# Kernel optimization log

Measured on AMD Instinct MI355X. Metric: run time of the kernel, lower is better.

Reference implementation:

```python
import jax, jax.numpy as jnp
import numpy as np

EMBED = 768
HEADS = 12
HDIM = EMBED // HEADS
FF = EMBED * 2
B, LQ, LK = 4, 2048, 2048


def _linear(x, W, b):
    # W: [in, out]
    return x @ W + b


def _layernorm(x, g, b, eps=1e-5):
    mu = jnp.mean(x, axis=-1, keepdims=True)
    var = jnp.mean(jnp.square(x - mu), axis=-1, keepdims=True)
    return (x - mu) * jax.lax.rsqrt(var + eps) * g + b


def _l2norm(x, eps=1e-12):
    # matches F.normalize: x / max(||x||_2, eps)
    n = jnp.sqrt(jnp.sum(jnp.square(x), axis=-1, keepdims=True))
    return x / jnp.maximum(n, eps)


def _heads(x):
    b, l, _ = x.shape
    return x.reshape(b, l, HEADS, HDIM).transpose(0, 2, 1, 3)  # [B,H,L,hd]


def setup_inputs() -> dict:
    key = jax.random.key(0)
    ks = jax.random.split(key, 20)
    s = 0.02
    d = {
        'image_tokens': jax.random.normal(ks[0], (B, LQ, EMBED), jnp.float32),
        'point_tokens': jax.random.normal(ks[1], (B, LK, EMBED), jnp.float32),
        'image_pos': jax.random.normal(ks[2], (B, LQ, EMBED), jnp.float32),
        'point_pos': jax.random.normal(ks[3], (B, LK, EMBED), jnp.float32),
        'Wip': jax.random.normal(ks[4], (EMBED, EMBED), jnp.float32) * s,
        'bip': jnp.zeros((EMBED,), jnp.float32),
        'Wpp': jax.random.normal(ks[5], (EMBED, EMBED), jnp.float32) * s,
        'bpp': jnp.zeros((EMBED,), jnp.float32),
        'Wq': jax.random.normal(ks[6], (EMBED, EMBED), jnp.float32) * s,
        'bq': jnp.zeros((EMBED,), jnp.float32),
        'Wk': jax.random.normal(ks[7], (EMBED, EMBED), jnp.float32) * s,
        'bk': jnp.zeros((EMBED,), jnp.float32),
        'Wv': jax.random.normal(ks[8], (EMBED, EMBED), jnp.float32) * s,
        'bv': jnp.zeros((EMBED,), jnp.float32),
        'Wo': jax.random.normal(ks[9], (EMBED, EMBED), jnp.float32) * s,
        'bo': jnp.zeros((EMBED,), jnp.float32),
        'g1': jnp.ones((EMBED,), jnp.float32),
        'b1': jnp.zeros((EMBED,), jnp.float32),
        'g2': jnp.ones((EMBED,), jnp.float32),
        'b2': jnp.zeros((EMBED,), jnp.float32),
        'Wf1': jax.random.normal(ks[10], (EMBED, FF), jnp.float32) * s,
        'bf1': jnp.zeros((FF,), jnp.float32),
        'Wf2': jax.random.normal(ks[11], (FF, EMBED), jnp.float32) * s,
        'bf2': jnp.zeros((EMBED,), jnp.float32),
    }
    return d


def reference(image_tokens, point_tokens, image_pos, point_pos,
              Wip, bip, Wpp, bpp, Wq, bq, Wk, bk, Wv, bv, Wo, bo,
              g1, b1, g2, b2, Wf1, bf1, Wf2, bf2):
    q = _linear(image_tokens + _linear(image_pos, Wip, bip), Wq, bq)
    k = _linear(point_tokens + _linear(point_pos, Wpp, bpp), Wk, bk)
    v = _linear(point_tokens, Wv, bv)

    q = _l2norm(_heads(q))  # [B,H,Lq,hd]
    k = _l2norm(_heads(k))  # [B,H,Lk,hd]
    v = _heads(v)           # [B,H,Lk,hd]

    scores = jnp.einsum('bhqd,bhkd->bhqk', q, k)
    attn = jax.nn.softmax(scores, axis=-1)
    fused = jnp.einsum('bhqk,bhkd->bhqd', attn, v)
    fused = fused.transpose(0, 2, 1, 3).reshape(image_tokens.shape[0], image_tokens.shape[1], EMBED)

    fused = _layernorm(image_tokens + _linear(fused, Wo, bo), g1, b1)
    h = _linear(fused, Wf1, bf1)
    h = 0.5 * h * (1.0 + jax.lax.erf(h / jnp.sqrt(jnp.float32(2.0))))  # exact GELU
    ff = _linear(h, Wf2, bf2)
    return _layernorm(fused + ff, g2, b2)
```

## Files before the change

kernel.cpp:

```cpp
#include <hip/hip_runtime.h>

#define EMBED 768
#define FFDIM 1536
#define BATCH 4
#define SEQ   2048
#define HEADS 12
#define MROWS (BATCH*SEQ)

typedef __attribute__((ext_vector_type(4))) float  f32x4;
typedef __attribute__((ext_vector_type(8))) __bf16 bf16x8;
typedef __attribute__((ext_vector_type(4))) short  s16x4;

__device__ __forceinline__ short f2bf(float f) {
    union { float f; unsigned u; } x; x.f = f;
    unsigned r = x.u + 0x7fffu + ((x.u >> 16) & 1u);
    return (short)(r >> 16);
}

__device__ __forceinline__ void gll16(const void* g, void* l) {
    __builtin_amdgcn_global_load_lds(
        (const __attribute__((address_space(1))) void*)g,
        (__attribute__((address_space(3))) void*)l, 16, 0, 0);
}

__global__ __launch_bounds__(256) void cvt4_kernel(
    const float* __restrict__ s0, const float* __restrict__ s1,
    const float* __restrict__ s2, const float* __restrict__ s3,
    short* __restrict__ o0, short* __restrict__ o1,
    short* __restrict__ o2, short* __restrict__ o3)
{
    const float* s; short* o;
    switch (blockIdx.y) {
        case 0:  s = s0; o = o0; break;
        case 1:  s = s1; o = o1; break;
        case 2:  s = s2; o = o2; break;
        default: s = s3; o = o3; break;
    }
    size_t i = ((size_t)blockIdx.x * 256 + threadIdx.x) * 4;
    float4 v = *(const float4*)(s + i);
    s16x4 r;
    r[0] = f2bf(v.x); r[1] = f2bf(v.y); r[2] = f2bf(v.z); r[3] = f2bf(v.w);
    *(s16x4*)(o + i) = r;
}

__global__ __launch_bounds__(256) void transpose_w(
    const float* __restrict__ W, short* __restrict__ Wt, int K, int N)
{
    __shared__ float tile[32][33];
    const int k0 = blockIdx.y * 32, n0 = blockIdx.x * 32;
    const int tx = threadIdx.x & 31, ty = threadIdx.x >> 5;
    #pragma unroll
    for (int i = 0; i < 32; i += 8)
        tile[ty + i][tx] = W[(size_t)(k0 + ty + i) * N + n0 + tx];
    __syncthreads();
    #pragma unroll
    for (int i = 0; i < 32; i += 8)
        Wt[(size_t)(n0 + ty + i) * K + k0 + tx] = f2bf(tile[tx][ty + i]);
}

__global__ __launch_bounds__(256) void transpose_v(
    const short* __restrict__ v, short* __restrict__ vt)
{
    __shared__ short tile[64][65];
    const int bh = blockIdx.y;
    const int b = bh / HEADS, h = bh % HEADS;
    const int k0 = blockIdx.x * 64;
    const int tx = threadIdx.x & 63, ty = threadIdx.x >> 6;
    #pragma unroll
    for (int i = 0; i < 64; i += 4)
        tile[ty + i][tx] = v[(size_t)(b * SEQ + k0 + ty + i) * EMBED + h * 64 + tx];
    __syncthreads();
    #pragma unroll
    for (int i = 0; i < 64; i += 4)
        vt[(size_t)(bh * 64 + ty + i) * SEQ + k0 + tx] = tile[tx][ty + i];
}

template<int L2N, int GELU_, int RES, int SBF, int SF32>
__global__ __launch_bounds__(256) void gemm_bt(
    const short* __restrict__ A, const short* __restrict__ Wt,
    const float* __restrict__ bias, const float* __restrict__ resid,
    short* __restrict__ outb, float* __restrict__ outf,
    int M, int N, int K)
{
    __shared__ short As[128][32];
    __shared__ short Bs[128][32];
    const int tid = threadIdx.x;
    const int mbase = blockIdx.y * 128, nbase = blockIdx.x * 128;
    const int wid = tid >> 6, lane = tid & 63;
    const int wm = wid >> 1, wn = wid & 1;
    const int l15 = lane & 15, lhi = lane >> 4;
    const int sr = tid >> 2;
    const int sc = (tid & 3) * 8;

    f32x4 acc[4][4] = {};

    const short* Ab = A  + (size_t)mbase * K;
    const short* Bb = Wt + (size_t)nbase * K;

    for (int k0 = 0; k0 < K; k0 += 32) {
        __syncthreads();
        gll16(Ab + (size_t)sr * K        + k0 + sc, &As[sr][sc]);
        gll16(Ab + (size_t)(64 + sr) * K + k0 + sc, &As[64 + sr][sc]);
        gll16(Bb + (size_t)sr * K        + k0 + sc, &Bs[sr][sc]);
        gll16(Bb + (size_t)(64 + sr) * K + k0 + sc, &Bs[64 + sr][sc]);
        __syncthreads();
        bf16x8 av[4], bv[4];
        #pragma unroll
        for (int t = 0; t < 4; ++t) {
            av[t] = *(const bf16x8*)(&As[wm * 64 + t * 16 + l15][lhi * 8]);
            bv[t] = *(const bf16x8*)(&Bs[wn * 64 + t * 16 + l15][lhi * 8]);
        }
        #pragma unroll
        for (int mt = 0; mt < 4; ++mt)
            #pragma unroll
            for (int nt = 0; nt < 4; ++nt)
                acc[mt][nt] = __builtin_amdgcn_mfma_f32_16x16x32_bf16(
                    av[mt], bv[nt], acc[mt][nt], 0, 0, 0);
    }

    #pragma unroll
    for (int mt = 0; mt < 4; ++mt) {
        float vals[4][4];
        #pragma unroll
        for (int nt = 0; nt < 4; ++nt) {
            const int col = nbase + wn * 64 + nt * 16 + l15;
            const float bc = bias[col];
            #pragma unroll
            for (int j = 0; j < 4; ++j) vals[nt][j] = acc[mt][nt][j] + bc;
        }
        if (RES) {
            #pragma unroll
            for (int nt = 0; nt < 4; ++nt) {
                const int col = nbase + wn * 64 + nt * 16 + l15;
                #pragma unroll
                for (int j = 0; j < 4; ++j) {
                    const int row = mbase + wm * 64 + mt * 16 + lhi * 4 + j;
                    vals[nt][j] += resid[(size_t)row * N + col];
                }
            }
        }
        if (L2N) {
            #pragma unroll
            for (int j = 0; j < 4; ++j) {
                float s = 0.f;
                #pragma unroll
                for (int nt = 0; nt < 4; ++nt) s += vals[nt][j] * vals[nt][j];
                s += __shfl_xor(s, 1); s += __shfl_xor(s, 2);
                s += __shfl_xor(s, 4); s += __shfl_xor(s, 8);
                const float inv = 1.0f / fmaxf(sqrtf(s), 1e-12f);
                #pragma unroll
                for (int nt = 0; nt < 4; ++nt) vals[nt][j] *= inv;
            }
        }
        if (GELU_) {
            #pragma unroll
            for (int nt = 0; nt < 4; ++nt)
                #pragma unroll
                for (int j = 0; j < 4; ++j) {
                    const float v = vals[nt][j];
                    vals[nt][j] = 0.5f * v * (1.0f + erff(v * 0.70710678118654752f));
                }
        }
        #pragma unroll
        for (int nt = 0; nt < 4; ++nt) {
            const int col = nbase + wn * 64 + nt * 16 + l15;
            #pragma unroll
            for (int j = 0; j < 4; ++j) {
                const int row = mbase + wm * 64 + mt * 16 + lhi * 4 + j;
                if (SBF)  outb[(size_t)row * N + col] = f2bf(vals[nt][j]);
                if (SF32) outf[(size_t)row * N + col] = vals[nt][j];
            }
        }
    }
}

__global__ __launch_bounds__(256) void attn_kernel(
    const short* __restrict__ qn, const short* __restrict__ kn,
    const short* __restrict__ vt, short* __restrict__ outp)
{
    __shared__ short Qs[64][64];
    __shared__ short Ks[64][64];
    __shared__ short Vs[64][64];
    __shared__ short Ps[64][64];

    const int bh = blockIdx.y;
    const int b = bh / HEADS, h = bh % HEADS;
    const int q0 = blockIdx.x * 64;
    const int tid = threadIdx.x, wid = tid >> 6, lane = tid & 63;
    const int l15 = lane & 15, lhi = lane >> 4;
    const int sr = tid >> 3;
    const int sc = (tid & 7) * 8;

    #pragma unroll
    for (int p = 0; p < 2; ++p) {
        const int r = p * 32 + sr;
        gll16(qn + (size_t)(b * SEQ + q0 + r) * EMBED + h * 64 + sc, &Qs[r][sc]);
    }

    f32x4 acc_o[4] = {};
    float rowsum[4] = {0.f, 0.f, 0.f, 0.f};

    for (int kt = 0; kt < SEQ / 64; ++kt) {
        const int k0 = kt * 64;
        __syncthreads();
        #pragma unroll
        for (int p = 0; p < 2; ++p) {
            const int r = p * 32 + sr;
            gll16(kn + (size_t)(b * SEQ + k0 + r) * EMBED + h * 64 + sc, &Ks[r][sc]);
            gll16(vt + (size_t)(bh * 64 + r) * SEQ + k0 + sc, &Vs[r][sc]);
        }
        __syncthreads();

        bf16x8 aq0 = *(const bf16x8*)(&Qs[wid * 16 + l15][lhi * 8]);
        bf16x8 aq1 = *(const bf16x8*)(&Qs[wid * 16 + l15][32 + lhi * 8]);
        #pragma unroll
        for (int nt = 0; nt < 4; ++nt) {
            bf16x8 bk0 = *(const bf16x8*)(&Ks[nt * 16 + l15][lhi * 8]);
            bf16x8 bk1 = *(const bf16x8*)(&Ks[nt * 16 + l15][32 + lhi * 8]);
            f32x4 s = {0.f, 0.f, 0.f, 0.f};
            s = __builtin_amdgcn_mfma_f32_16x16x32_bf16(aq0, bk0, s, 0, 0, 0);
            s = __builtin_amdgcn_mfma_f32_16x16x32_bf16(aq1, bk1, s, 0, 0, 0);
            #pragma unroll
            for (int j = 0; j < 4; ++j) {
                const float e = __expf(s[j]);
                rowsum[j] += e;
                Ps[wid * 16 + lhi * 4 + j][nt * 16 + l15] = f2bf(e);
            }
        }
        __syncthreads();

        #pragma unroll
        for (int ks = 0; ks < 2; ++ks) {
            bf16x8 ap = *(const bf16x8*)(&Ps[wid * 16 + l15][ks * 32 + lhi * 8]);
            #pragma unroll
            for (int dt = 0; dt < 4; ++dt) {
                bf16x8 bvv = *(const bf16x8*)(&Vs[dt * 16 + l15][ks * 32 + lhi * 8]);
                acc_o[dt] = __builtin_amdgcn_mfma_f32_16x16x32_bf16(ap, bvv, acc_o[dt], 0, 0, 0);
            }
        }
    }

    #pragma unroll
    for (int j = 0; j < 4; ++j) {
        float s = rowsum[j];
        s += __shfl_xor(s, 1); s += __shfl_xor(s, 2);
        s += __shfl_xor(s, 4); s += __shfl_xor(s, 8);
        rowsum[j] = s;
    }

    #pragma unroll
    for (int dt = 0; dt < 4; ++dt)
        #pragma unroll
        for (int j = 0; j < 4; ++j) {
            const int row = q0 + wid * 16 + lhi * 4 + j;
            const int col = h * 64 + dt * 16 + l15;
            outp[(size_t)(b * SEQ + row) * EMBED + col] = f2bf(acc_o[dt][j] / rowsum[j]);
        }
}

template<int SBF>
__global__ __launch_bounds__(256) void layernorm_768(
    const float* __restrict__ x, const float* __restrict__ g, const float* __restrict__ bb,
    float* __restrict__ outf, short* __restrict__ outb)
{
    const int row = blockIdx.x;
    const float* xr = x + (size_t)row * EMBED;
    const int t = threadIdx.x;
    const float v0 = xr[t], v1 = xr[t + 256], v2 = xr[t + 512];
    float s = v0 + v1 + v2;
    #pragma unroll
    for (int m = 1; m < 64; m <<= 1) s += __shfl_xor(s, m);
    __shared__ float red[4];
    __shared__ float red2[4];
    const int wid = t >> 6, lane = t & 63;
    if (lane == 0) red[wid] = s;
    __syncthreads();
    const float mu = (red[0] + red[1] + red[2] + red[3]) * (1.0f / 768.0f);
    const float d0 = v0 - mu, d1 = v1 - mu, d2 = v2 - mu;
    float ss = d0 * d0 + d1 * d1 + d2 * d2;
    #pragma unroll
    for (int m = 1; m < 64; m <<= 1) ss += __shfl_xor(ss, m);
    if (lane == 0) red2[wid] = ss;
    __syncthreads();
    const float var = (red2[0] + red2[1] + red2[2] + red2[3]) * (1.0f / 768.0f);
    const float inv = rsqrtf(var + 1e-5f);
    const float y0 = d0 * inv * g[t] + bb[t];
    const float y1 = d1 * inv * g[t + 256] + bb[t + 256];
    const float y2 = d2 * inv * g[t + 512] + bb[t + 512];
    float* of = outf + (size_t)row * EMBED;
    of[t] = y0; of[t + 256] = y1; of[t + 512] = y2;
    if (SBF) {
        short* ob = outb + (size_t)row * EMBED;
        ob[t] = f2bf(y0); ob[t + 256] = f2bf(y1); ob[t + 512] = f2bf(y2);
    }
}

extern "C" void kernel_launch(void* const* d_in, const int* in_sizes, int n_in,
                              void* d_out, int out_size, void* d_ws, size_t ws_size,
                              hipStream_t stream)
{
    (void)in_sizes; (void)n_in; (void)out_size; (void)ws_size;
    const float* itok = (const float*)d_in[0];
    const float* ptok = (const float*)d_in[1];
    const float* ipos = (const float*)d_in[2];
    const float* ppos = (const float*)d_in[3];
    const float* Wip = (const float*)d_in[4];  const float* bip = (const float*)d_in[5];
    const float* Wpp = (const float*)d_in[6];  const float* bpp = (const float*)d_in[7];
    const float* Wq  = (const float*)d_in[8];  const float* bq  = (const float*)d_in[9];
    const float* Wk  = (const float*)d_in[10]; const float* bk  = (const float*)d_in[11];
    const float* Wv  = (const float*)d_in[12]; const float* bv  = (const float*)d_in[13];
    const float* Wo  = (const float*)d_in[14]; const float* bo  = (const float*)d_in[15];
    const float* g1  = (const float*)d_in[16]; const float* b1  = (const float*)d_in[17];
    const float* g2  = (const float*)d_in[18]; const float* b2  = (const float*)d_in[19];
    const float* Wf1 = (const float*)d_in[20]; const float* bf1 = (const float*)d_in[21];
    const float* Wf2 = (const float*)d_in[22]; const float* bf2 = (const float*)d_in[23];
    float* out = (float*)d_out;

    char* ws = (char*)d_ws;
    constexpr size_t SZ_BF  = (size_t)MROWS * EMBED * 2;
    constexpr size_t SZ_F32 = (size_t)MROWS * EMBED * 4;
    constexpr size_t W768B  = (size_t)EMBED * EMBED * 2;
    constexpr size_t W1536B = (size_t)EMBED * FFDIM * 2;

    size_t o = 0;
    short* it_bf    = (short*)(ws + o); o += SZ_BF;
    short* pt_bf    = (short*)(ws + o); o += SZ_BF;
    short* ip_bf    = (short*)(ws + o); o += SZ_BF;
    short* pp_bf    = (short*)(ws + o); o += SZ_BF;
    short* qin_bf   = (short*)(ws + o); o += SZ_BF;
    short* kin_bf   = (short*)(ws + o); o += SZ_BF;
    short* qn_bf    = (short*)(ws + o); o += SZ_BF;
    short* kn_bf    = (short*)(ws + o); o += SZ_BF;
    short* attn_bf  = (short*)(ws + o); o += SZ_BF;
    float* x_f32    = (float*)(ws + o); o += SZ_F32;
    short* fused_bf = (short*)(ws + o); o += SZ_BF;
    float* fused_f32= (float*)(ws + o); o += SZ_F32;
    short* wip_t = (short*)(ws + o); o += W768B;
    short* wpp_t = (short*)(ws + o); o += W768B;
    short* wq_t  = (short*)(ws + o); o += W768B;
    short* wk_t  = (short*)(ws + o); o += W768B;
    short* wv_t  = (short*)(ws + o); o += W768B;
    short* wo_t  = (short*)(ws + o); o += W768B;
    short* wf1_t = (short*)(ws + o); o += W1536B;
    short* wf2_t = (short*)(ws + o); o += W1536B;
    short* v_bf  = ip_bf;
    short* vt_bf = pp_bf;
    short* h_bf  = qin_bf;

    const dim3 blk(256);

    cvt4_kernel<<<dim3(MROWS * EMBED / 1024, 4), blk, 0, stream>>>(
        itok, ptok, ipos, ppos, it_bf, pt_bf, ip_bf, pp_bf);

    transpose_w<<<dim3(EMBED / 32, EMBED / 32), blk, 0, stream>>>(Wip, wip_t, EMBED, EMBED);
    transpose_w<<<dim3(EMBED / 32, EMBED / 32), blk, 0, stream>>>(Wpp, wpp_t, EMBED, EMBED);
    transpose_w<<<dim3(EMBED / 32, EMBED / 32), blk, 0, stream>>>(Wq,  wq_t,  EMBED, EMBED);
    transpose_w<<<dim3(EMBED / 32, EMBED / 32), blk, 0, stream>>>(Wk,  wk_t,  EMBED, EMBED);
    transpose_w<<<dim3(EMBED / 32, EMBED / 32), blk, 0, stream>>>(Wv,  wv_t,  EMBED, EMBED);
    transpose_w<<<dim3(EMBED / 32, EMBED / 32), blk, 0, stream>>>(Wo,  wo_t,  EMBED, EMBED);
    transpose_w<<<dim3(FFDIM / 32, EMBED / 32), blk, 0, stream>>>(Wf1, wf1_t, EMBED, FFDIM);
    transpose_w<<<dim3(EMBED / 32, FFDIM / 32), blk, 0, stream>>>(Wf2, wf2_t, FFDIM, EMBED);

    const dim3 g768(EMBED / 128, MROWS / 128);
    const dim3 g1536(FFDIM / 128, MROWS / 128);

    gemm_bt<0,0,1,1,0><<<g768, blk, 0, stream>>>(ip_bf, wip_t, bip, itok, qin_bf, nullptr, MROWS, EMBED, EMBED);
    gemm_bt<0,0,1,1,0><<<g768, blk, 0, stream>>>(pp_bf, wpp_t, bpp, ptok, kin_bf, nullptr, MROWS, EMBED, EMBED);
    gemm_bt<1,0,0,1,0><<<g768, blk, 0, stream>>>(qin_bf, wq_t, bq, nullptr, qn_bf, nullptr, MROWS, EMBED, EMBED);
    gemm_bt<1,0,0,1,0><<<g768, blk, 0, stream>>>(kin_bf, wk_t, bk, nullptr, kn_bf, nullptr, MROWS, EMBED, EMBED);
    gemm_bt<0,0,0,1,0><<<g768, blk, 0, stream>>>(pt_bf, wv_t, bv, nullptr, v_bf, nullptr, MROWS, EMBED, EMBED);

    transpose_v<<<dim3(SEQ / 64, BATCH * HEADS), blk, 0, stream>>>(v_bf, vt_bf);
    attn_kernel<<<dim3(SEQ / 64, BATCH * HEADS), blk, 0, stream>>>(qn_bf, kn_bf, vt_bf, attn_bf);

    gemm_bt<0,0,1,0,1><<<g768, blk, 0, stream>>>(attn_bf, wo_t, bo, itok, nullptr, x_f32, MROWS, EMBED, EMBED);
    layernorm_768<1><<<dim3(MROWS), blk, 0, stream>>>(x_f32, g1, b1, fused_f32, fused_bf);
    gemm_bt<0,1,0,1,0><<<g1536, blk, 0, stream>>>(fused_bf, wf1_t, bf1, nullptr, h_bf, nullptr, MROWS, FFDIM, EMBED);
    gemm_bt<0,0,1,0,1><<<g768, blk, 0, stream>>>(h_bf, wf2_t, bf2, fused_f32, nullptr, x_f32, MROWS, EMBED, FFDIM);
    layernorm_768<0><<<dim3(MROWS), blk, 0, stream>>>(x_f32, g2, b2, out, nullptr);
}
```

Before: 640.5 us.

## Double-buffer GEMM and attention LDS tiles and swizzle attention shared memory

The GEMM main loop now keeps two LDS stages and prefetches the next K slice while computing the current one, with one barrier per iteration instead of two. The attention kernel moves to 512 threads handling 128 query rows per block. It double-buffers the K and V tiles, hoists the Q fragments out of the loop, and drops the barrier around the per-wave P tile. Attention LDS accesses for Q, K, V and P use an XOR chunk swizzle meant to avoid bank conflicts. The cost is twice the LDS footprint per block and correctness that depends on the async global-to-LDS loads finishing before each barrier.

```diff
diff --git a/kernel.cpp b/kernel.cpp
--- a/kernel.cpp
+++ b/kernel.cpp
@@ -23,6 +23,10 @@
         (__attribute__((address_space(3))) void*)l, 16, 0, 0);
 }
 
+__device__ __forceinline__ bf16x8 ldsw(const short* base, int row, int chunk) {
+    return *(const bf16x8*)((const char*)base + row * 128 + (((chunk ^ (row & 7))) << 4));
+}
+
 __global__ __launch_bounds__(256) void cvt4_kernel(
     const float* __restrict__ s0, const float* __restrict__ s1,
     const float* __restrict__ s2, const float* __restrict__ s3,
@@ -82,8 +86,8 @@
     short* __restrict__ outb, float* __restrict__ outf,
     int M, int N, int K)
 {
-    __shared__ short As[128][32];
-    __shared__ short Bs[128][32];
+    __shared__ short As[2][128][32];
+    __shared__ short Bs[2][128][32];
     const int tid = threadIdx.x;
     const int mbase = blockIdx.y * 128, nbase = blockIdx.x * 128;
     const int wid = tid >> 6, lane = tid & 63;
@@ -97,18 +101,24 @@
     const short* Ab = A  + (size_t)mbase * K;
     const short* Bb = Wt + (size_t)nbase * K;
 
-    for (int k0 = 0; k0 < K; k0 += 32) {
-        __syncthreads();
-        gll16(Ab + (size_t)sr * K        + k0 + sc, &As[sr][sc]);
-        gll16(Ab + (size_t)(64 + sr) * K + k0 + sc, &As[64 + sr][sc]);
-        gll16(Bb + (size_t)sr * K        + k0 + sc, &Bs[sr][sc]);
-        gll16(Bb + (size_t)(64 + sr) * K + k0 + sc, &Bs[64 + sr][sc]);
-        __syncthreads();
+#define GSTAGE(buf, kk)                                                         \
+    gll16(Ab + (size_t)sr * K        + (kk) + sc, &As[buf][sr][sc]);            \
+    gll16(Ab + (size_t)(64 + sr) * K + (kk) + sc, &As[buf][64 + sr][sc]);       \
+    gll16(Bb + (size_t)sr * K        + (kk) + sc, &Bs[buf][sr][sc]);            \
+    gll16(Bb + (size_t)(64 + sr) * K + (kk) + sc, &Bs[buf][64 + sr][sc]);
+
+    GSTAGE(0, 0);
+    __syncthreads();
+
+    const int nk = K >> 5;
+    for (int t = 0; t < nk; ++t) {
+        const int cur = t & 1;
+        if (t + 1 < nk) { GSTAGE(cur ^ 1, (t + 1) << 5); }
         bf16x8 av[4], bv[4];
         #pragma unroll
-        for (int t = 0; t < 4; ++t) {
-            av[t] = *(const bf16x8*)(&As[wm * 64 + t * 16 + l15][lhi * 8]);
-            bv[t] = *(const bf16x8*)(&Bs[wn * 64 + t * 16 + l15][lhi * 8]);
+        for (int tt = 0; tt < 4; ++tt) {
+            av[tt] = *(const bf16x8*)(&As[cur][wm * 64 + tt * 16 + l15][lhi * 8]);
+            bv[tt] = *(const bf16x8*)(&Bs[cur][wn * 64 + tt * 16 + l15][lhi * 8]);
         }
         #pragma unroll
         for (int mt = 0; mt < 4; ++mt)
@@ -116,7 +126,9 @@
             for (int nt = 0; nt < 4; ++nt)
                 acc[mt][nt] = __builtin_amdgcn_mfma_f32_16x16x32_bf16(
                     av[mt], bv[nt], acc[mt][nt], 0, 0, 0);
-    }
+        __syncthreads();
+    }
+#undef GSTAGE
 
     #pragma unroll
     for (int mt = 0; mt < 4; ++mt) {
@@ -174,49 +186,57 @@
     }
 }
 
-__global__ __launch_bounds__(256) void attn_kernel(
+__global__ __launch_bounds__(512) void attn_kernel(
     const short* __restrict__ qn, const short* __restrict__ kn,
     const short* __restrict__ vt, short* __restrict__ outp)
 {
-    __shared__ short Qs[64][64];
-    __shared__ short Ks[64][64];
-    __shared__ short Vs[64][64];
-    __shared__ short Ps[64][64];
+    __shared__ short Qs[128][64];
+    __shared__ short Ks[2][64][64];
+    __shared__ short Vs[2][64][64];
+    __shared__ short Ps[128][64];
 
     const int bh = blockIdx.y;
     const int b = bh / HEADS, h = bh % HEADS;
-    const int q0 = blockIdx.x * 64;
+    const int q0 = blockIdx.x * 128;
     const int tid = threadIdx.x, wid = tid >> 6, lane = tid & 63;
     const int l15 = lane & 15, lhi = lane >> 4;
-    const int sr = tid >> 3;
-    const int sc = (tid & 7) * 8;
+    const int srow = tid >> 3;
+    const int schk = tid & 7;
 
     #pragma unroll
     for (int p = 0; p < 2; ++p) {
-        const int r = p * 32 + sr;
-        gll16(qn + (size_t)(b * SEQ + q0 + r) * EMBED + h * 64 + sc, &Qs[r][sc]);
-    }
+        const int cid = p * 512 + tid;
+        const int r = cid >> 3, c = cid & 7;
+        gll16(qn + (size_t)(b * SEQ + q0 + r) * EMBED + h * 64 + ((c ^ (r & 7)) * 8),
+              &Qs[r][c * 8]);
+    }
+    gll16(kn + (size_t)(b * SEQ + srow) * EMBED + h * 64 + ((schk ^ (srow & 7)) * 8),
+          &Ks[0][srow][schk * 8]);
+    gll16(vt + (size_t)(bh * 64 + srow) * SEQ + ((schk ^ (srow & 7)) * 8),
+          &Vs[0][srow][schk * 8]);
+    __syncthreads();
+
+    const bf16x8 aq0 = ldsw(&Qs[0][0], wid * 16 + l15, lhi);
+    const bf16x8 aq1 = ldsw(&Qs[0][0], wid * 16 + l15, 4 + lhi);
 
     f32x4 acc_o[4] = {};
     float rowsum[4] = {0.f, 0.f, 0.f, 0.f};
+    char* const ps_base = (char*)&Ps[0][0];
 
     for (int kt = 0; kt < SEQ / 64; ++kt) {
-        const int k0 = kt * 64;
-        __syncthreads();
-        #pragma unroll
-        for (int p = 0; p < 2; ++p) {
-            const int r = p * 32 + sr;
-            gll16(kn + (size_t)(b * SEQ + k0 + r) * EMBED + h * 64 + sc, &Ks[r][sc]);
-            gll16(vt + (size_t)(bh * 64 + r) * SEQ + k0 + sc, &Vs[r][sc]);
-        }
-        __syncthreads();
-
-        bf16x8 aq0 = *(const bf16x8*)(&Qs[wid * 16 + l15][lhi * 8]);
-        bf16x8 aq1 = *(const bf16x8*)(&Qs[wid * 16 + l15][32 + lhi * 8]);
+        const int cur = kt & 1;
+        if (kt + 1 < SEQ / 64) {
+            const int k0n = (kt + 1) * 64;
+            gll16(kn + (size_t)(b * SEQ + k0n + srow) * EMBED + h * 64 + ((schk ^ (srow & 7)) * 8),
+                  &Ks[cur ^ 1][srow][schk * 8]);
+            gll16(vt + (size_t)(bh * 64 + srow) * SEQ + k0n + ((schk ^ (srow & 7)) * 8),
+                  &Vs[cur ^ 1][srow][schk * 8]);
+        }
+
         #pragma unroll
         for (int nt = 0; nt < 4; ++nt) {
-            bf16x8 bk0 = *(const bf16x8*)(&Ks[nt * 16 + l15][lhi * 8]);
-            bf16x8 bk1 = *(const bf16x8*)(&Ks[nt * 16 + l15][32 + lhi * 8]);
+            bf16x8 bk0 = ldsw(&Ks[cur][0][0], nt * 16 + l15, lhi);
+            bf16x8 bk1 = ldsw(&Ks[cur][0][0], nt * 16 + l15, 4 + lhi);
             f32x4 s = {0.f, 0.f, 0.f, 0.f};
             s = __builtin_amdgcn_mfma_f32_16x16x32_bf16(aq0, bk0, s, 0, 0, 0);
             s = __builtin_amdgcn_mfma_f32_16x16x32_bf16(aq1, bk1, s, 0, 0, 0);
@@ -224,20 +244,23 @@
             for (int j = 0; j < 4; ++j) {
                 const float e = __expf(s[j]);
                 rowsum[j] += e;
-                Ps[wid * 16 + lhi * 4 + j][nt * 16 + l15] = f2bf(e);
+                const int q = wid * 16 + lhi * 4 + j;
+                const int k = nt * 16 + l15;
+                const int chunk = k >> 3;
+                *(short*)(ps_base + q * 128 + ((chunk ^ (q & 7)) << 4) + (k & 7) * 2) = f2bf(e);
             }
         }
-        __syncthreads();
 
         #pragma unroll
         for (int ks = 0; ks < 2; ++ks) {
-            bf16x8 ap = *(const bf16x8*)(&Ps[wid * 16 + l15][ks * 32 + lhi * 8]);
+            bf16x8 ap = ldsw(&Ps[0][0], wid * 16 + l15, ks * 4 + lhi);
             #pragma unroll
             for (int dt = 0; dt < 4; ++dt) {
-                bf16x8 bvv = *(const bf16x8*)(&Vs[dt * 16 + l15][ks * 32 + lhi * 8]);
+                bf16x8 bvv = ldsw(&Vs[cur][0][0], dt * 16 + l15, ks * 4 + lhi);
                 acc_o[dt] = __builtin_amdgcn_mfma_f32_16x16x32_bf16(ap, bvv, acc_o[dt], 0, 0, 0);
             }
         }
+        __syncthreads();
     }
 
     #pragma unroll
@@ -371,7 +394,7 @@
     gemm_bt<0,0,0,1,0><<<g768, blk, 0, stream>>>(pt_bf, wv_t, bv, nullptr, v_bf, nullptr, MROWS, EMBED, EMBED);
 
     transpose_v<<<dim3(SEQ / 64, BATCH * HEADS), blk, 0, stream>>>(v_bf, vt_bf);
-    attn_kernel<<<dim3(SEQ / 64, BATCH * HEADS), blk, 0, stream>>>(qn_bf, kn_bf, vt_bf, attn_bf);
+    attn_kernel<<<dim3(SEQ / 128, BATCH * HEADS), dim3(512), 0, stream>>>(qn_bf, kn_bf, vt_bf, attn_bf);
 
     gemm_bt<0,0,1,0,1><<<g768, blk, 0, stream>>>(attn_bf, wo_t, bo, itok, nullptr, x_f32, MROWS, EMBED, EMBED);
     layernorm_768<1><<<dim3(MROWS), blk, 0, stream>>>(x_f32, g1, b1, fused_f32, fused_bf);
```

After: 561.3 us. -12.4%, faster.
